# Optimization experiments

Hardware: AMD Instinct MI355X
Metric: run time of the kernel (lower is better)

Reference implementation:

```python
import jax, jax.numpy as jnp
import numpy as np

B, V, J, H, W = 32, 2, 17, 128, 128
TEMP = 0.05   # SoftArgmax2D softmax_temp
EPS = 1e-12


def _soft_argmax(hm):
    # hm: (B*V, J, H, W) -> homogeneous coords (B*V, 3, J), per-joint max value
    bv, j, h, w = hm.shape
    p = jax.nn.softmax(hm.reshape(bv, j, h * w) / TEMP, axis=-1).reshape(bv, j, h, w)
    xs = jnp.arange(w, dtype=hm.dtype)
    ys = jnp.arange(h, dtype=hm.dtype)
    x = jnp.einsum('bjhw,w->bj', p, xs)
    y = jnp.einsum('bjhw,h->bj', p, ys)
    coords = jnp.stack([x, y, jnp.ones_like(x)], axis=1)  # (bv, 3, j)
    maxv = hm.max(axis=(-2, -1))
    return coords, maxv


def _skew(t):
    # t: (..., 3) -> skew-symmetric (..., 3, 3), matches -t_mat^T + t_mat in source
    tx, ty, tz = t[..., 0], t[..., 1], t[..., 2]
    z = jnp.zeros_like(tx)
    return jnp.stack([jnp.stack([z, -tz, ty], -1),
                      jnp.stack([tz, z, -tx], -1),
                      jnp.stack([-ty, tx, z], -1)], -2)


def _forward(origin_hms, AP_K, AP_T, LAT_K, LAT_T):
    K = jnp.stack([AP_K, LAT_K], axis=1)              # (B,V,3,3)
    T = jnp.stack([AP_T, LAT_T], axis=1)              # (B,V,4,4)
    R = T[:, :, :3, :3]
    t_std = T[:, :, :3, 3]                            # (B,V,3) standard_cam_T

    # fundamental matrices for all ordered pairs: cam1 = view j, cam2 = view i
    r = jnp.einsum('bimk,bjnk->bijmn', R, R)          # R_i @ R_j^T
    t = t_std[:, :, None, :] - jnp.einsum('bijmn,bjn->bijm', r, t_std)
    M = jnp.einsum('bijmn,bijnk->bijmk', _skew(t), r)
    invK = jnp.linalg.inv(K)
    # F = invK_i^T @ [t]x @ r @ invK_j
    F = jnp.einsum('bipm,bijpq,bjql->bijml', invK, M, invK)  # (B,V,V,3,3)

    coords, maxv = _soft_argmax(origin_hms)           # (B*V,3,J), (B*V,J)
    inv_aff = jnp.diag(jnp.asarray([4.0, 4.0, 1.0], dtype=origin_hms.dtype))  # inverse of 0.25 scale
    img = jnp.einsum('mn,bvnj->bvmj', inv_aff, coords.reshape(B, V, 3, J))
    confi = maxv.reshape(B, V, J)

    # epipolar distances, fully vectorized over (b, i, j) pairs
    l = jnp.einsum('bijmn,bjnk->bijmk', F, img)       # epipolar lines in view i from joints of view j
    cv = img[:, :, None]                              # (B,V,1,3,J)
    num = jnp.sum(cv * l, axis=3) ** 2                # (B,V,V,J)
    lp = jnp.einsum('bijnm,bink->bijmk', F, img)      # F^T @ cv_joints
    div = l[..., 0, :] ** 2 + l[..., 1, :] ** 2 + lp[..., 0, :] ** 2 + lp[..., 1, :] ** 2
    dist_full = jnp.sqrt(num / (div + EPS))           # (B,V,V,J)

    others = np.asarray([[j for j in range(V) if j != i] for i in range(V)])  # (V,V-1)
    ii = np.repeat(np.arange(V)[:, None], V - 1, axis=1)
    distances = dist_full[:, ii, others]              # (B,V,V-1,J)

    # stand-in for ViewWeightNet: confidence minus mean epipolar error, softmax over views
    score = confi - distances.mean(axis=2)            # (B,V,J)
    vw = jax.nn.softmax(score, axis=1)                # (B,V,J)

    mv = jnp.where(maxv > 0.01, maxv, 1e6).reshape(B * V, J, 1, 1)
    hms_norm = origin_hms / mv
    hm4 = hms_norm.reshape(B, V, J, H, W)

    # cat order: self heatmap first, then other views (matches get_warp_weight / cat_hm layout)
    order = np.asarray([[i] + [j for j in range(V) if j != i] for i in range(V)])  # (V,V)
    cat_hm = hm4[:, order]                            # (B,V,V,J,H,W); identity-warp stand-in for CamFusionModule
    ww = vw[:, order]                                 # (B,V,V,J) warp weights
    fused_hm = jnp.sum(ww[..., None, None] * cat_hm, axis=2).reshape(B * V, J, H, W)

    coords2, _ = _soft_argmax(fused_hm)
    img2 = jnp.einsum('mn,bvnj->bvmj', inv_aff, coords2.reshape(B, V, 3, J))
    return img2[:, :, :2, :], fused_hm


def setup_inputs() -> dict:
    key = jax.random.key(0)
    k1, k2, k3, k4, k5 = jax.random.split(key, 5)
    hms = jax.random.uniform(k1, (B * V, J, H, W), dtype=jnp.float32)

    def make_K(k):
        f = 1000.0 + jax.random.normal(k, (B,)) * 10.0
        Km = jnp.zeros((B, 3, 3), dtype=jnp.float32)
        Km = Km.at[:, 0, 0].set(f).at[:, 1, 1].set(f)
        Km = Km.at[:, 0, 2].set(256.0).at[:, 1, 2].set(256.0).at[:, 2, 2].set(1.0)
        return Km

    def make_T(k):
        A = jax.random.normal(k, (B, 3, 3))
        Q, _ = jnp.linalg.qr(A)
        Q = Q * jnp.linalg.det(Q)[:, None, None]  # force det = +1 (proper rotation)
        t = jax.random.normal(jax.random.fold_in(k, 1), (B, 3, 1)) * 0.1 + jnp.asarray([0.0, 0.0, 5.0]).reshape(3, 1)
        bottom = jnp.tile(jnp.asarray([[[0.0, 0.0, 0.0, 1.0]]]), (B, 1, 1))
        return jnp.concatenate([jnp.concatenate([Q, t], axis=2), bottom], axis=1).astype(jnp.float32)

    return {"origin_hms": hms, "AP_K": make_K(k2), "AP_T": make_T(k3),
            "LAT_K": make_K(k4), "LAT_T": make_T(k5)}


def reference(origin_hms, AP_K, AP_T, LAT_K, LAT_T):
    return _forward(origin_hms, AP_K, AP_T, LAT_K, LAT_T)
```

## Files before the change

kernel.cpp:

```cpp
#include <hip/hip_runtime.h>
#include <math.h>

#define NB 32
#define NV 2
#define NJ 17
#define NH 128
#define NW 128
#define MAPN (NH * NW)
#define MAPN4 (MAPN / 4)
#define NMAPS (NB * NV * NJ)
#define NBJ (NB * NJ)
#define OUT0N (NB * NV * 2 * NJ)
#define INV_TEMP 20.0f
#define EPS_D 1e-12f

#define S_CHUNKS 4
#define S_F4 (MAPN4 / S_CHUNKS)
#define F_CHUNKS 8
#define F_F4 (MAPN4 / F_CHUNKS)

#define WS_STATS_B (NMAPS * S_CHUNKS * 16)
#define WS_W_B (NBJ * 2 * 4)
#define WS_F_B (NBJ * F_CHUNKS * 16)
#define WS_NEEDED (WS_STATS_B + WS_W_B + WS_F_B)

typedef float vfloat4 __attribute__((ext_vector_type(4)));

__device__ __forceinline__ float waveMax(float v) {
#pragma unroll
    for (int off = 32; off > 0; off >>= 1)
        v = fmaxf(v, __shfl_xor(v, off, 64));
    return v;
}
__device__ __forceinline__ float waveSum(float v) {
#pragma unroll
    for (int off = 32; off > 0; off >>= 1)
        v += __shfl_xor(v, off, 64);
    return v;
}

__device__ __forceinline__ void inv3(const float K[3][3], float o[3][3]) {
    const float a = K[0][0], b = K[0][1], c = K[0][2];
    const float d = K[1][0], e = K[1][1], f = K[1][2];
    const float g = K[2][0], h = K[2][1], i = K[2][2];
    const float A =  (e * i - f * h);
    const float Bv = -(d * i - f * g);
    const float C =  (d * h - e * g);
    const float det = a * A + b * Bv + c * C;
    const float id = 1.0f / det;
    o[0][0] = A * id;  o[0][1] = -(b * i - c * h) * id;  o[0][2] = (b * f - c * e) * id;
    o[1][0] = Bv * id; o[1][1] = (a * i - c * g) * id;   o[1][2] = -(a * f - c * d) * id;
    o[2][0] = C * id;  o[2][1] = -(a * h - b * g) * id;  o[2][2] = (a * e - b * d) * id;
}

__global__ __launch_bounds__(256, 4) void k_stats(const float* __restrict__ hms,
                                                  float* __restrict__ ws) {
    const int blk = blockIdx.x;
    const int mi = blk >> 2, c = blk & 3;
    const int tid = threadIdx.x, wid = tid >> 6, lane = tid & 63;
    const float4* A = (const float4*)hms + (size_t)mi * MAPN4 + (size_t)c * S_F4;

    float mx = -1e30f, s = 0.f, sx = 0.f, sy = 0.f;
#pragma unroll
    for (int k = 0; k < 4; ++k) {
        const int i4 = tid + k * 256;
        const float4 v = A[i4];
        const int e0 = (c * S_F4 + i4) * 4;
        const float hh = (float)(e0 >> 7);
        const float ww = (float)(e0 & 127);
        mx = fmaxf(mx, fmaxf(fmaxf(v.x, v.y), fmaxf(v.z, v.w)));
        const float ea = __expf((v.x - 1.0f) * INV_TEMP);
        const float eb = __expf((v.y - 1.0f) * INV_TEMP);
        const float ec = __expf((v.z - 1.0f) * INV_TEMP);
        const float ed = __expf((v.w - 1.0f) * INV_TEMP);
        const float se = (ea + eb) + (ec + ed);
        s += se; sy += se * hh;
        sx += ea * ww + eb * (ww + 1.f) + ec * (ww + 2.f) + ed * (ww + 3.f);
    }

    mx = waveMax(mx); s = waveSum(s); sx = waveSum(sx); sy = waveSum(sy);
    __shared__ float red[4][4];
    if (lane == 0) { red[0][wid] = mx; red[1][wid] = s; red[2][wid] = sx; red[3][wid] = sy; }
    __syncthreads();
    if (tid == 0) {
        float M = red[0][0], S = red[1][0], SX = red[2][0], SY = red[3][0];
#pragma unroll
        for (int w = 1; w < 4; ++w) {
            M = fmaxf(M, red[0][w]); S += red[1][w]; SX += red[2][w]; SY += red[3][w];
        }
        ((float4*)ws)[blk] = make_float4(M, S, SX, SY);
    }
}

__global__ void k_weights(const float* __restrict__ ws_stats,
                          const float* __restrict__ APK, const float* __restrict__ APT,
                          const float* __restrict__ LATK, const float* __restrict__ LATT,
                          float* __restrict__ wsw) {
    const int bj = blockIdx.x * 64 + threadIdx.x;
    if (bj >= NBJ) return;
    const int b = bj / NJ, j = bj % NJ;

    float conf[2], img[2][3];
    const float4* st = (const float4*)ws_stats;
#pragma unroll
    for (int v = 0; v < 2; ++v) {
        const int mi = (b * 2 + v) * NJ + j;
        float M = -1e30f, S = 0.f, SX = 0.f, SY = 0.f;
#pragma unroll
        for (int c = 0; c < S_CHUNKS; ++c) {
            const float4 p = st[mi * S_CHUNKS + c];
            M = fmaxf(M, p.x); S += p.y; SX += p.z; SY += p.w;
        }
        conf[v] = M;
        img[v][0] = 4.0f * (SX / S);
        img[v][1] = 4.0f * (SY / S);
        img[v][2] = 1.0f;
    }

    float F[2][3][3];
    {
        float Km[2][3][3], R[2][3][3], tr[2][3], iK[2][3][3];
        for (int r = 0; r < 3; ++r)
            for (int cc = 0; cc < 3; ++cc) {
                Km[0][r][cc] = APK[b * 9 + r * 3 + cc];
                Km[1][r][cc] = LATK[b * 9 + r * 3 + cc];
                R[0][r][cc] = APT[b * 16 + r * 4 + cc];
                R[1][r][cc] = LATT[b * 16 + r * 4 + cc];
            }
        for (int r = 0; r < 3; ++r) {
            tr[0][r] = APT[b * 16 + r * 4 + 3];
            tr[1][r] = LATT[b * 16 + r * 4 + 3];
        }
        inv3(Km[0], iK[0]);
        inv3(Km[1], iK[1]);

        for (int i = 0; i < 2; ++i) {
            const int jj = 1 - i;
            float r[3][3];
            for (int m = 0; m < 3; ++m)
                for (int n = 0; n < 3; ++n)
                    r[m][n] = R[i][m][0] * R[jj][n][0] + R[i][m][1] * R[jj][n][1] + R[i][m][2] * R[jj][n][2];
            float tv[3];
            for (int m = 0; m < 3; ++m)
                tv[m] = tr[i][m] - (r[m][0] * tr[jj][0] + r[m][1] * tr[jj][1] + r[m][2] * tr[jj][2]);
            const float S[3][3] = {{0.f, -tv[2], tv[1]}, {tv[2], 0.f, -tv[0]}, {-tv[1], tv[0], 0.f}};
            float M[3][3];
            for (int m = 0; m < 3; ++m)
                for (int n = 0; n < 3; ++n)
                    M[m][n] = S[m][0] * r[0][n] + S[m][1] * r[1][n] + S[m][2] * r[2][n];
            float tmp[3][3];
            for (int p = 0; p < 3; ++p)
                for (int l = 0; l < 3; ++l)
                    tmp[p][l] = M[p][0] * iK[jj][0][l] + M[p][1] * iK[jj][1][l] + M[p][2] * iK[jj][2][l];
            for (int m = 0; m < 3; ++m)
                for (int l = 0; l < 3; ++l)
                    F[i][m][l] = iK[i][0][m] * tmp[0][l] + iK[i][1][m] * tmp[1][l] + iK[i][2][m] * tmp[2][l];
        }
    }

    float score[2];
#pragma unroll
    for (int i = 0; i < 2; ++i) {
        const int jj = 1 - i;
        const float l0 = F[i][0][0] * img[jj][0] + F[i][0][1] * img[jj][1] + F[i][0][2] * img[jj][2];
        const float l1 = F[i][1][0] * img[jj][0] + F[i][1][1] * img[jj][1] + F[i][1][2] * img[jj][2];
        const float l2 = F[i][2][0] * img[jj][0] + F[i][2][1] * img[jj][1] + F[i][2][2] * img[jj][2];
        const float sdot = img[i][0] * l0 + img[i][1] * l1 + img[i][2] * l2;
        const float num = sdot * sdot;
        const float lp0 = F[i][0][0] * img[i][0] + F[i][1][0] * img[i][1] + F[i][2][0] * img[i][2];
        const float lp1 = F[i][0][1] * img[i][0] + F[i][1][1] * img[i][1] + F[i][2][1] * img[i][2];
        const float dv = l0 * l0 + l1 * l1 + lp0 * lp0 + lp1 * lp1;
        score[i] = conf[i] - sqrtf(num / (dv + EPS_D));
    }
    const float mS = fmaxf(score[0], score[1]);
    const float e0w = __expf(score[0] - mS), e1w = __expf(score[1] - mS);
    const float inv = 1.0f / (e0w + e1w);
    const float mv0 = conf[0] > 0.01f ? conf[0] : 1e6f;
    const float mv1 = conf[1] > 0.01f ? conf[1] : 1e6f;
    wsw[bj * 2 + 0] = (e0w * inv) / mv0;
    wsw[bj * 2 + 1] = (e1w * inv) / mv1;
}

__global__ __launch_bounds__(256, 4) void k_fuse(const float* __restrict__ hms,
                                                 const float* __restrict__ wsw,
                                                 float* __restrict__ out,
                                                 float* __restrict__ wsf) {
    const int blk = blockIdx.x;
    const int bj = blk >> 3, c = blk & 7;
    const int b = bj / NJ, j = bj % NJ;
    const int tid = threadIdx.x, wid = tid >> 6, lane = tid & 63;

    const float w0 = wsw[bj * 2 + 0];
    const float w1 = wsw[bj * 2 + 1];

    const size_t m0 = ((size_t)(b * 2 + 0) * NJ + j) * MAPN4;
    const size_t m1 = ((size_t)(b * 2 + 1) * NJ + j) * MAPN4;
    const float4* A  = (const float4*)hms + m0 + (size_t)c * F_F4;
    const float4* Bp = (const float4*)hms + m1 + (size_t)c * F_F4;
    float* outhm = out + OUT0N;
    vfloat4* O0 = reinterpret_cast<vfloat4*>(outhm) + m0 + (size_t)c * F_F4;
    vfloat4* O1 = reinterpret_cast<vfloat4*>(outhm) + m1 + (size_t)c * F_F4;

    float s = 0.f, sx = 0.f, sy = 0.f;
#pragma unroll
    for (int k = 0; k < 2; ++k) {
        const int i4 = tid + k * 256;
        const float4 a = A[i4];
        const float4 cc = Bp[i4];
        vfloat4 f;
        f.x = w0 * a.x + w1 * cc.x;
        f.y = w0 * a.y + w1 * cc.y;
        f.z = w0 * a.z + w1 * cc.z;
        f.w = w0 * a.w + w1 * cc.w;
        __builtin_nontemporal_store(f, &O0[i4]);
        __builtin_nontemporal_store(f, &O1[i4]);
        const int e0 = (c * F_F4 + i4) * 4;
        const float hh = (float)(e0 >> 7);
        const float ww = (float)(e0 & 127);
        const float ea = __expf((f.x - 1.0f) * INV_TEMP);
        const float eb = __expf((f.y - 1.0f) * INV_TEMP);
        const float ec = __expf((f.z - 1.0f) * INV_TEMP);
        const float ed = __expf((f.w - 1.0f) * INV_TEMP);
        const float se = (ea + eb) + (ec + ed);
        s += se; sy += se * hh;
        sx += ea * ww + eb * (ww + 1.f) + ec * (ww + 2.f) + ed * (ww + 3.f);
    }

    s = waveSum(s); sx = waveSum(sx); sy = waveSum(sy);
    __shared__ float red[3][4];
    if (lane == 0) { red[0][wid] = s; red[1][wid] = sx; red[2][wid] = sy; }
    __syncthreads();
    if (tid == 0) {
        float S = red[0][0], SX = red[1][0], SY = red[2][0];
#pragma unroll
        for (int w = 1; w < 4; ++w) { S += red[0][w]; SX += red[1][w]; SY += red[2][w]; }
        ((float4*)wsf)[blk] = make_float4(S, SX, SY, 0.f);
    }
}

__global__ void k_out(const float* __restrict__ wsf, float* __restrict__ out) {
    const int bj = blockIdx.x * 64 + threadIdx.x;
    if (bj >= NBJ) return;
    const int b = bj / NJ, j = bj % NJ;
    const float4* p = (const float4*)wsf + bj * F_CHUNKS;
    float S = 0.f, SX = 0.f, SY = 0.f;
#pragma unroll
    for (int c = 0; c < F_CHUNKS; ++c) {
        const float4 q = p[c];
        S += q.x; SX += q.y; SY += q.z;
    }
    const float x4 = 4.0f * (SX / S);
    const float y4 = 4.0f * (SY / S);
    out[((b * 2 + 0) * 2 + 0) * NJ + j] = x4;
    out[((b * 2 + 0) * 2 + 1) * NJ + j] = y4;
    out[((b * 2 + 1) * 2 + 0) * NJ + j] = x4;
    out[((b * 2 + 1) * 2 + 1) * NJ + j] = y4;
}

__global__ __launch_bounds__(512, 2) void k_one(const float* __restrict__ hms,
                                                const float* __restrict__ APK,
                                                const float* __restrict__ APT,
                                                const float* __restrict__ LATK,
                                                const float* __restrict__ LATT,
                                                float* __restrict__ out) {
    const int blk = blockIdx.x;
    const int b = blk / NJ, j = blk % NJ;
    const int tid = threadIdx.x;
    const int wid = tid >> 6, lane = tid & 63;

    float F[2][3][3];
    {
        float Km[2][3][3], R[2][3][3], tr[2][3], iK[2][3][3];
        for (int r = 0; r < 3; ++r)
            for (int c = 0; c < 3; ++c) {
                Km[0][r][c] = APK[b * 9 + r * 3 + c];
                Km[1][r][c] = LATK[b * 9 + r * 3 + c];
                R[0][r][c] = APT[b * 16 + r * 4 + c];
                R[1][r][c] = LATT[b * 16 + r * 4 + c];
            }
        for (int r = 0; r < 3; ++r) {
            tr[0][r] = APT[b * 16 + r * 4 + 3];
            tr[1][r] = LATT[b * 16 + r * 4 + 3];
        }
        inv3(Km[0], iK[0]);
        inv3(Km[1], iK[1]);

        for (int i = 0; i < 2; ++i) {
            const int jj = 1 - i;
            float r[3][3];
            for (int m = 0; m < 3; ++m)
                for (int n = 0; n < 3; ++n)
                    r[m][n] = R[i][m][0] * R[jj][n][0] + R[i][m][1] * R[jj][n][1] + R[i][m][2] * R[jj][n][2];
            float tv[3];
            for (int m = 0; m < 3; ++m)
                tv[m] = tr[i][m] - (r[m][0] * tr[jj][0] + r[m][1] * tr[jj][1] + r[m][2] * tr[jj][2]);
            const float S[3][3] = {{0.f, -tv[2], tv[1]}, {tv[2], 0.f, -tv[0]}, {-tv[1], tv[0], 0.f}};
            float M[3][3];
            for (int m = 0; m < 3; ++m)
                for (int n = 0; n < 3; ++n)
                    M[m][n] = S[m][0] * r[0][n] + S[m][1] * r[1][n] + S[m][2] * r[2][n];
            float tmp[3][3];
            for (int p = 0; p < 3; ++p)
                for (int l = 0; l < 3; ++l)
                    tmp[p][l] = M[p][0] * iK[jj][0][l] + M[p][1] * iK[jj][1][l] + M[p][2] * iK[jj][2][l];
            for (int m = 0; m < 3; ++m)
                for (int l = 0; l < 3; ++l)
                    F[i][m][l] = iK[i][0][m] * tmp[0][l] + iK[i][1][m] * tmp[1][l] + iK[i][2][m] * tmp[2][l];
        }
    }

    const int idx0 = (b * 2 + 0) * NJ + j;
    const int idx1 = (b * 2 + 1) * NJ + j;
    const size_t m0 = (size_t)idx0 * MAPN4;
    const size_t m1 = (size_t)idx1 * MAPN4;
    const float4* A  = (const float4*)hms + m0;
    const float4* Bp = (const float4*)hms + m1;

    float4 va[8];
    float mx0 = -1e30f, s0 = 0.f, sx0 = 0.f, sy0 = 0.f;
    float mx1 = -1e30f, s1 = 0.f, sx1 = 0.f, sy1 = 0.f;
#pragma unroll
    for (int u = 0; u < 8; ++u) {
        const int i4 = tid + u * 512;
        const float4 v = A[i4];
        const float4 w = Bp[i4];
        va[u] = v;
        const int e0 = i4 * 4;
        const float hh = (float)(e0 >> 7);
        const float ww = (float)(e0 & 127);
        {
            mx0 = fmaxf(mx0, fmaxf(fmaxf(v.x, v.y), fmaxf(v.z, v.w)));
            const float ea = __expf((v.x - 1.0f) * INV_TEMP);
            const float eb = __expf((v.y - 1.0f) * INV_TEMP);
            const float ec = __expf((v.z - 1.0f) * INV_TEMP);
            const float ed = __expf((v.w - 1.0f) * INV_TEMP);
            const float se = (ea + eb) + (ec + ed);
            s0 += se; sy0 += se * hh;
            sx0 += ea * ww + eb * (ww + 1.f) + ec * (ww + 2.f) + ed * (ww + 3.f);
        }
        {
            mx1 = fmaxf(mx1, fmaxf(fmaxf(w.x, w.y), fmaxf(w.z, w.w)));
            const float ea = __expf((w.x - 1.0f) * INV_TEMP);
            const float eb = __expf((w.y - 1.0f) * INV_TEMP);
            const float ec = __expf((w.z - 1.0f) * INV_TEMP);
            const float ed = __expf((w.w - 1.0f) * INV_TEMP);
            const float se = (ea + eb) + (ec + ed);
            s1 += se; sy1 += se * hh;
            sx1 += ea * ww + eb * (ww + 1.f) + ec * (ww + 2.f) + ed * (ww + 3.f);
        }
    }

    __shared__ float red[8][8];
    mx0 = waveMax(mx0); mx1 = waveMax(mx1);
    s0 = waveSum(s0); sx0 = waveSum(sx0); sy0 = waveSum(sy0);
    s1 = waveSum(s1); sx1 = waveSum(sx1); sy1 = waveSum(sy1);
    if (lane == 0) {
        red[0][wid] = mx0; red[1][wid] = s0; red[2][wid] = sx0; red[3][wid] = sy0;
        red[4][wid] = mx1; red[5][wid] = s1; red[6][wid] = sx1; red[7][wid] = sy1;
    }
    __syncthreads();
    float M0 = red[0][0], S0 = red[1][0], SX0 = red[2][0], SY0 = red[3][0];
    float M1 = red[4][0], S1 = red[5][0], SX1 = red[6][0], SY1 = red[7][0];
#pragma unroll
    for (int w = 1; w < 8; ++w) {
        M0 = fmaxf(M0, red[0][w]); S0 += red[1][w]; SX0 += red[2][w]; SY0 += red[3][w];
        M1 = fmaxf(M1, red[4][w]); S1 += red[5][w]; SX1 += red[6][w]; SY1 += red[7][w];
    }

    float w0, w1;
    {
        const float conf[2] = {M0, M1};
        float img[2][3];
        img[0][0] = 4.0f * (SX0 / S0); img[0][1] = 4.0f * (SY0 / S0); img[0][2] = 1.0f;
        img[1][0] = 4.0f * (SX1 / S1); img[1][1] = 4.0f * (SY1 / S1); img[1][2] = 1.0f;

        float score[2];
        for (int i = 0; i < 2; ++i) {
            const int jj = 1 - i;
            const float l0 = F[i][0][0] * img[jj][0] + F[i][0][1] * img[jj][1] + F[i][0][2] * img[jj][2];
            const float l1 = F[i][1][0] * img[jj][0] + F[i][1][1] * img[jj][1] + F[i][1][2] * img[jj][2];
            const float l2 = F[i][2][0] * img[jj][0] + F[i][2][1] * img[jj][1] + F[i][2][2] * img[jj][2];
            const float sdot = img[i][0] * l0 + img[i][1] * l1 + img[i][2] * l2;
            const float num = sdot * sdot;
            const float lp0 = F[i][0][0] * img[i][0] + F[i][1][0] * img[i][1] + F[i][2][0] * img[i][2];
            const float lp1 = F[i][0][1] * img[i][0] + F[i][1][1] * img[i][1] + F[i][2][1] * img[i][2];
            const float dv = l0 * l0 + l1 * l1 + lp0 * lp0 + lp1 * lp1;
            score[i] = conf[i] - sqrtf(num / (dv + EPS_D));
        }
        const float mS = fmaxf(score[0], score[1]);
        const float e0w = __expf(score[0] - mS), e1w = __expf(score[1] - mS);
        const float inv = 1.0f / (e0w + e1w);
        const float mv0 = conf[0] > 0.01f ? conf[0] : 1e6f;
        const float mv1 = conf[1] > 0.01f ? conf[1] : 1e6f;
        w0 = (e0w * inv) / mv0;
        w1 = (e1w * inv) / mv1;
    }

    float* outhm = out + OUT0N;
    vfloat4* O0 = reinterpret_cast<vfloat4*>(outhm) + m0;
    vfloat4* O1 = reinterpret_cast<vfloat4*>(outhm) + m1;

    float s = 0.f, sx = 0.f, sy = 0.f;
#pragma unroll
    for (int u = 0; u < 8; ++u) {
        const int i4 = tid + u * 512;
        const float4 a = va[u];
        const float4 c = Bp[i4];
        vfloat4 f;
        f.x = w0 * a.x + w1 * c.x;
        f.y = w0 * a.y + w1 * c.y;
        f.z = w0 * a.z + w1 * c.z;
        f.w = w0 * a.w + w1 * c.w;
        __builtin_nontemporal_store(f, &O0[i4]);
        __builtin_nontemporal_store(f, &O1[i4]);
        const int e0 = i4 * 4;
        const float hh = (float)(e0 >> 7);
        const float ww = (float)(e0 & 127);
        const float ea = __expf((f.x - 1.0f) * INV_TEMP);
        const float eb = __expf((f.y - 1.0f) * INV_TEMP);
        const float ec = __expf((f.z - 1.0f) * INV_TEMP);
        const float ed = __expf((f.w - 1.0f) * INV_TEMP);
        const float se = (ea + eb) + (ec + ed);
        s += se; sy += se * hh;
        sx += ea * ww + eb * (ww + 1.f) + ec * (ww + 2.f) + ed * (ww + 3.f);
    }

    __syncthreads();
    s = waveSum(s); sx = waveSum(sx); sy = waveSum(sy);
    if (lane == 0) { red[0][wid] = s; red[1][wid] = sx; red[2][wid] = sy; }
    __syncthreads();
    if (tid == 0) {
        float S = red[0][0], SX = red[1][0], SY = red[2][0];
#pragma unroll
        for (int w = 1; w < 8; ++w) { S += red[0][w]; SX += red[1][w]; SY += red[2][w]; }
        const float x4 = 4.0f * (SX / S);
        const float y4 = 4.0f * (SY / S);
        out[((b * 2 + 0) * 2 + 0) * NJ + j] = x4;
        out[((b * 2 + 0) * 2 + 1) * NJ + j] = y4;
        out[((b * 2 + 1) * 2 + 0) * NJ + j] = x4;
        out[((b * 2 + 1) * 2 + 1) * NJ + j] = y4;
    }
}

extern "C" void kernel_launch(void* const* d_in, const int* in_sizes, int n_in,
                              void* d_out, int out_size, void* d_ws, size_t ws_size,
                              hipStream_t stream) {
    const float* hms  = (const float*)d_in[0];
    const float* APK  = (const float*)d_in[1];
    const float* APT  = (const float*)d_in[2];
    const float* LATK = (const float*)d_in[3];
    const float* LATT = (const float*)d_in[4];
    float* out = (float*)d_out;

    if (d_ws != nullptr && ws_size >= (size_t)WS_NEEDED) {
        float* ws_stats = (float*)d_ws;
        float* ws_w = ws_stats + NMAPS * S_CHUNKS * 4;
        float* ws_f = ws_w + NBJ * 2;
        k_stats<<<NMAPS * S_CHUNKS, 256, 0, stream>>>(hms, ws_stats);
        k_weights<<<(NBJ + 63) / 64, 64, 0, stream>>>(ws_stats, APK, APT, LATK, LATT, ws_w);
        k_fuse<<<NBJ * F_CHUNKS, 256, 0, stream>>>(hms, ws_w, out, ws_f);
        k_out<<<(NBJ + 63) / 64, 64, 0, stream>>>(ws_f, out);
    } else {
        k_one<<<NBJ, 512, 0, stream>>>(hms, APK, APT, LATK, LATT, out);
    }
}
```

Baseline: 141.9 us.

## Fuse stats, weights and fusion passes into one kernel split by halves

```diff
diff --git a/kernel.cpp b/kernel.cpp
--- a/kernel.cpp
+++ b/kernel.cpp
@@ -8,21 +8,13 @@
 #define NW 128
 #define MAPN (NH * NW)
 #define MAPN4 (MAPN / 4)
-#define NMAPS (NB * NV * NJ)
 #define NBJ (NB * NJ)
 #define OUT0N (NB * NV * 2 * NJ)
 #define INV_TEMP 20.0f
 #define EPS_D 1e-12f
 
-#define S_CHUNKS 4
-#define S_F4 (MAPN4 / S_CHUNKS)
-#define F_CHUNKS 8
-#define F_F4 (MAPN4 / F_CHUNKS)
-
-#define WS_STATS_B (NMAPS * S_CHUNKS * 16)
-#define WS_W_B (NBJ * 2 * 4)
-#define WS_F_B (NBJ * F_CHUNKS * 16)
-#define WS_NEEDED (WS_STATS_B + WS_W_B + WS_F_B)
+#define HALF4 (MAPN4 / 2)
+#define WS_NEEDED (NBJ * 2 * 16)
 
 typedef float vfloat4 __attribute__((ext_vector_type(4)));
 
@@ -53,218 +45,16 @@
     o[2][0] = C * id;  o[2][1] = -(a * h - b * g) * id;  o[2][2] = (a * e - b * d) * id;
 }
 
-__global__ __launch_bounds__(256, 4) void k_stats(const float* __restrict__ hms,
-                                                  float* __restrict__ ws) {
+__global__ __launch_bounds__(512, 2) void k_main(const float* __restrict__ hms,
+                                                 const float* __restrict__ APK,
+                                                 const float* __restrict__ APT,
+                                                 const float* __restrict__ LATK,
+                                                 const float* __restrict__ LATT,
+                                                 float* __restrict__ ws_fp,
+                                                 float* __restrict__ out) {
     const int blk = blockIdx.x;
-    const int mi = blk >> 2, c = blk & 3;
-    const int tid = threadIdx.x, wid = tid >> 6, lane = tid & 63;
-    const float4* A = (const float4*)hms + (size_t)mi * MAPN4 + (size_t)c * S_F4;
-
-    float mx = -1e30f, s = 0.f, sx = 0.f, sy = 0.f;
-#pragma unroll
-    for (int k = 0; k < 4; ++k) {
-        const int i4 = tid + k * 256;
-        const float4 v = A[i4];
-        const int e0 = (c * S_F4 + i4) * 4;
-        const float hh = (float)(e0 >> 7);
-        const float ww = (float)(e0 & 127);
-        mx = fmaxf(mx, fmaxf(fmaxf(v.x, v.y), fmaxf(v.z, v.w)));
-        const float ea = __expf((v.x - 1.0f) * INV_TEMP);
-        const float eb = __expf((v.y - 1.0f) * INV_TEMP);
-        const float ec = __expf((v.z - 1.0f) * INV_TEMP);
-        const float ed = __expf((v.w - 1.0f) * INV_TEMP);
-        const float se = (ea + eb) + (ec + ed);
-        s += se; sy += se * hh;
-        sx += ea * ww + eb * (ww + 1.f) + ec * (ww + 2.f) + ed * (ww + 3.f);
-    }
-
-    mx = waveMax(mx); s = waveSum(s); sx = waveSum(sx); sy = waveSum(sy);
-    __shared__ float red[4][4];
-    if (lane == 0) { red[0][wid] = mx; red[1][wid] = s; red[2][wid] = sx; red[3][wid] = sy; }
-    __syncthreads();
-    if (tid == 0) {
-        float M = red[0][0], S = red[1][0], SX = red[2][0], SY = red[3][0];
-#pragma unroll
-        for (int w = 1; w < 4; ++w) {
-            M = fmaxf(M, red[0][w]); S += red[1][w]; SX += red[2][w]; SY += red[3][w];
-        }
-        ((float4*)ws)[blk] = make_float4(M, S, SX, SY);
-    }
-}
-
-__global__ void k_weights(const float* __restrict__ ws_stats,
-                          const float* __restrict__ APK, const float* __restrict__ APT,
-                          const float* __restrict__ LATK, const float* __restrict__ LATT,
-                          float* __restrict__ wsw) {
-    const int bj = blockIdx.x * 64 + threadIdx.x;
-    if (bj >= NBJ) return;
+    const int bj = blk >> 1, half = blk & 1;
     const int b = bj / NJ, j = bj % NJ;
-
-    float conf[2], img[2][3];
-    const float4* st = (const float4*)ws_stats;
-#pragma unroll
-    for (int v = 0; v < 2; ++v) {
-        const int mi = (b * 2 + v) * NJ + j;
-        float M = -1e30f, S = 0.f, SX = 0.f, SY = 0.f;
-#pragma unroll
-        for (int c = 0; c < S_CHUNKS; ++c) {
-            const float4 p = st[mi * S_CHUNKS + c];
-            M = fmaxf(M, p.x); S += p.y; SX += p.z; SY += p.w;
-        }
-        conf[v] = M;
-        img[v][0] = 4.0f * (SX / S);
-        img[v][1] = 4.0f * (SY / S);
-        img[v][2] = 1.0f;
-    }
-
-    float F[2][3][3];
-    {
-        float Km[2][3][3], R[2][3][3], tr[2][3], iK[2][3][3];
-        for (int r = 0; r < 3; ++r)
-            for (int cc = 0; cc < 3; ++cc) {
-                Km[0][r][cc] = APK[b * 9 + r * 3 + cc];
-                Km[1][r][cc] = LATK[b * 9 + r * 3 + cc];
-                R[0][r][cc] = APT[b * 16 + r * 4 + cc];
-                R[1][r][cc] = LATT[b * 16 + r * 4 + cc];
-            }
-        for (int r = 0; r < 3; ++r) {
-            tr[0][r] = APT[b * 16 + r * 4 + 3];
-            tr[1][r] = LATT[b * 16 + r * 4 + 3];
-        }
-        inv3(Km[0], iK[0]);
-        inv3(Km[1], iK[1]);
-
-        for (int i = 0; i < 2; ++i) {
-            const int jj = 1 - i;
-            float r[3][3];
-            for (int m = 0; m < 3; ++m)
-                for (int n = 0; n < 3; ++n)
-                    r[m][n] = R[i][m][0] * R[jj][n][0] + R[i][m][1] * R[jj][n][1] + R[i][m][2] * R[jj][n][2];
-            float tv[3];
-            for (int m = 0; m < 3; ++m)
-                tv[m] = tr[i][m] - (r[m][0] * tr[jj][0] + r[m][1] * tr[jj][1] + r[m][2] * tr[jj][2]);
-            const float S[3][3] = {{0.f, -tv[2], tv[1]}, {tv[2], 0.f, -tv[0]}, {-tv[1], tv[0], 0.f}};
-            float M[3][3];
-            for (int m = 0; m < 3; ++m)
-                for (int n = 0; n < 3; ++n)
-                    M[m][n] = S[m][0] * r[0][n] + S[m][1] * r[1][n] + S[m][2] * r[2][n];
-            float tmp[3][3];
-            for (int p = 0; p < 3; ++p)
-                for (int l = 0; l < 3; ++l)
-                    tmp[p][l] = M[p][0] * iK[jj][0][l] + M[p][1] * iK[jj][1][l] + M[p][2] * iK[jj][2][l];
-            for (int m = 0; m < 3; ++m)
-                for (int l = 0; l < 3; ++l)
-                    F[i][m][l] = iK[i][0][m] * tmp[0][l] + iK[i][1][m] * tmp[1][l] + iK[i][2][m] * tmp[2][l];
-        }
-    }
-
-    float score[2];
-#pragma unroll
-    for (int i = 0; i < 2; ++i) {
-        const int jj = 1 - i;
-        const float l0 = F[i][0][0] * img[jj][0] + F[i][0][1] * img[jj][1] + F[i][0][2] * img[jj][2];
-        const float l1 = F[i][1][0] * img[jj][0] + F[i][1][1] * img[jj][1] + F[i][1][2] * img[jj][2];
-        const float l2 = F[i][2][0] * img[jj][0] + F[i][2][1] * img[jj][1] + F[i][2][2] * img[jj][2];
-        const float sdot = img[i][0] * l0 + img[i][1] * l1 + img[i][2] * l2;
-        const float num = sdot * sdot;
-        const float lp0 = F[i][0][0] * img[i][0] + F[i][1][0] * img[i][1] + F[i][2][0] * img[i][2];
-        const float lp1 = F[i][0][1] * img[i][0] + F[i][1][1] * img[i][1] + F[i][2][1] * img[i][2];
-        const float dv = l0 * l0 + l1 * l1 + lp0 * lp0 + lp1 * lp1;
-        score[i] = conf[i] - sqrtf(num / (dv + EPS_D));
-    }
-    const float mS = fmaxf(score[0], score[1]);
-    const float e0w = __expf(score[0] - mS), e1w = __expf(score[1] - mS);
-    const float inv = 1.0f / (e0w + e1w);
-    const float mv0 = conf[0] > 0.01f ? conf[0] : 1e6f;
-    const float mv1 = conf[1] > 0.01f ? conf[1] : 1e6f;
-    wsw[bj * 2 + 0] = (e0w * inv) / mv0;
-    wsw[bj * 2 + 1] = (e1w * inv) / mv1;
-}
-
-__global__ __launch_bounds__(256, 4) void k_fuse(const float* __restrict__ hms,
-                                                 const float* __restrict__ wsw,
-                                                 float* __restrict__ out,
-                                                 float* __restrict__ wsf) {
-    const int blk = blockIdx.x;
-    const int bj = blk >> 3, c = blk & 7;
-    const int b = bj / NJ, j = bj % NJ;
-    const int tid = threadIdx.x, wid = tid >> 6, lane = tid & 63;
-
-    const float w0 = wsw[bj * 2 + 0];
-    const float w1 = wsw[bj * 2 + 1];
-
-    const size_t m0 = ((size_t)(b * 2 + 0) * NJ + j) * MAPN4;
-    const size_t m1 = ((size_t)(b * 2 + 1) * NJ + j) * MAPN4;
-    const float4* A  = (const float4*)hms + m0 + (size_t)c * F_F4;
-    const float4* Bp = (const float4*)hms + m1 + (size_t)c * F_F4;
-    float* outhm = out + OUT0N;
-    vfloat4* O0 = reinterpret_cast<vfloat4*>(outhm) + m0 + (size_t)c * F_F4;
-    vfloat4* O1 = reinterpret_cast<vfloat4*>(outhm) + m1 + (size_t)c * F_F4;
-
-    float s = 0.f, sx = 0.f, sy = 0.f;
-#pragma unroll
-    for (int k = 0; k < 2; ++k) {
-        const int i4 = tid + k * 256;
-        const float4 a = A[i4];
-        const float4 cc = Bp[i4];
-        vfloat4 f;
-        f.x = w0 * a.x + w1 * cc.x;
-        f.y = w0 * a.y + w1 * cc.y;
-        f.z = w0 * a.z + w1 * cc.z;
-        f.w = w0 * a.w + w1 * cc.w;
-        __builtin_nontemporal_store(f, &O0[i4]);
-        __builtin_nontemporal_store(f, &O1[i4]);
-        const int e0 = (c * F_F4 + i4) * 4;
-        const float hh = (float)(e0 >> 7);
-        const float ww = (float)(e0 & 127);
-        const float ea = __expf((f.x - 1.0f) * INV_TEMP);
-        const float eb = __expf((f.y - 1.0f) * INV_TEMP);
-        const float ec = __expf((f.z - 1.0f) * INV_TEMP);
-        const float ed = __expf((f.w - 1.0f) * INV_TEMP);
-        const float se = (ea + eb) + (ec + ed);
-        s += se; sy += se * hh;
-        sx += ea * ww + eb * (ww + 1.f) + ec * (ww + 2.f) + ed * (ww + 3.f);
-    }
-
-    s = waveSum(s); sx = waveSum(sx); sy = waveSum(sy);
-    __shared__ float red[3][4];
-    if (lane == 0) { red[0][wid] = s; red[1][wid] = sx; red[2][wid] = sy; }
-    __syncthreads();
-    if (tid == 0) {
-        float S = red[0][0], SX = red[1][0], SY = red[2][0];
-#pragma unroll
-        for (int w = 1; w < 4; ++w) { S += red[0][w]; SX += red[1][w]; SY += red[2][w]; }
-        ((float4*)wsf)[blk] = make_float4(S, SX, SY, 0.f);
-    }
-}
-
-__global__ void k_out(const float* __restrict__ wsf, float* __restrict__ out) {
-    const int bj = blockIdx.x * 64 + threadIdx.x;
-    if (bj >= NBJ) return;
-    const int b = bj / NJ, j = bj % NJ;
-    const float4* p = (const float4*)wsf + bj * F_CHUNKS;
-    float S = 0.f, SX = 0.f, SY = 0.f;
-#pragma unroll
-    for (int c = 0; c < F_CHUNKS; ++c) {
-        const float4 q = p[c];
-        S += q.x; SX += q.y; SY += q.z;
-    }
-    const float x4 = 4.0f * (SX / S);
-    const float y4 = 4.0f * (SY / S);
-    out[((b * 2 + 0) * 2 + 0) * NJ + j] = x4;
-    out[((b * 2 + 0) * 2 + 1) * NJ + j] = y4;
-    out[((b * 2 + 1) * 2 + 0) * NJ + j] = x4;
-    out[((b * 2 + 1) * 2 + 1) * NJ + j] = y4;
-}
-
-__global__ __launch_bounds__(512, 2) void k_one(const float* __restrict__ hms,
-                                                const float* __restrict__ APK,
-                                                const float* __restrict__ APT,
-                                                const float* __restrict__ LATK,
-                                                const float* __restrict__ LATT,
-                                                float* __restrict__ out) {
-    const int blk = blockIdx.x;
-    const int b = blk / NJ, j = blk % NJ;
     const int tid = threadIdx.x;
     const int wid = tid >> 6, lane = tid & 63;
 
@@ -309,10 +99,199 @@
         }
     }
 
-    const int idx0 = (b * 2 + 0) * NJ + j;
-    const int idx1 = (b * 2 + 1) * NJ + j;
-    const size_t m0 = (size_t)idx0 * MAPN4;
-    const size_t m1 = (size_t)idx1 * MAPN4;
+    const size_t m0 = ((size_t)(b * 2 + 0) * NJ + j) * MAPN4;
+    const size_t m1 = ((size_t)(b * 2 + 1) * NJ + j) * MAPN4;
+    const float4* A  = (const float4*)hms + m0;
+    const float4* Bp = (const float4*)hms + m1;
+
+    float mx0 = -1e30f, s0 = 0.f, sx0 = 0.f, sy0 = 0.f;
+    float mx1 = -1e30f, s1 = 0.f, sx1 = 0.f, sy1 = 0.f;
+#pragma unroll
+    for (int u = 0; u < 8; ++u) {
+        const int i4 = tid + u * 512;
+        const float4 v = A[i4];
+        const float4 w = Bp[i4];
+        const int e0 = i4 * 4;
+        const float hh = (float)(e0 >> 7);
+        const float ww = (float)(e0 & 127);
+        {
+            mx0 = fmaxf(mx0, fmaxf(fmaxf(v.x, v.y), fmaxf(v.z, v.w)));
+            const float ea = __expf((v.x - 1.0f) * INV_TEMP);
+            const float eb = __expf((v.y - 1.0f) * INV_TEMP);
+            const float ec = __expf((v.z - 1.0f) * INV_TEMP);
+            const float ed = __expf((v.w - 1.0f) * INV_TEMP);
+            const float se = (ea + eb) + (ec + ed);
+            s0 += se; sy0 += se * hh;
+            sx0 += ea * ww + eb * (ww + 1.f) + ec * (ww + 2.f) + ed * (ww + 3.f);
+        }
+        {
+            mx1 = fmaxf(mx1, fmaxf(fmaxf(w.x, w.y), fmaxf(w.z, w.w)));
+            const float ea = __expf((w.x - 1.0f) * INV_TEMP);
+            const float eb = __expf((w.y - 1.0f) * INV_TEMP);
+            const float ec = __expf((w.z - 1.0f) * INV_TEMP);
+            const float ed = __expf((w.w - 1.0f) * INV_TEMP);
+            const float se = (ea + eb) + (ec + ed);
+            s1 += se; sy1 += se * hh;
+            sx1 += ea * ww + eb * (ww + 1.f) + ec * (ww + 2.f) + ed * (ww + 3.f);
+        }
+    }
+
+    __shared__ float red[8][8];
+    mx0 = waveMax(mx0); mx1 = waveMax(mx1);
+    s0 = waveSum(s0); sx0 = waveSum(sx0); sy0 = waveSum(sy0);
+    s1 = waveSum(s1); sx1 = waveSum(sx1); sy1 = waveSum(sy1);
+    if (lane == 0) {
+        red[0][wid] = mx0; red[1][wid] = s0; red[2][wid] = sx0; red[3][wid] = sy0;
+        red[4][wid] = mx1; red[5][wid] = s1; red[6][wid] = sx1; red[7][wid] = sy1;
+    }
+    __syncthreads();
+    float M0 = red[0][0], S0 = red[1][0], SX0 = red[2][0], SY0 = red[3][0];
+    float M1 = red[4][0], S1 = red[5][0], SX1 = red[6][0], SY1 = red[7][0];
+#pragma unroll
+    for (int w = 1; w < 8; ++w) {
+        M0 = fmaxf(M0, red[0][w]); S0 += red[1][w]; SX0 += red[2][w]; SY0 += red[3][w];
+        M1 = fmaxf(M1, red[4][w]); S1 += red[5][w]; SX1 += red[6][w]; SY1 += red[7][w];
+    }
+
+    float w0, w1;
+    {
+        const float conf[2] = {M0, M1};
+        float img[2][3];
+        img[0][0] = 4.0f * (SX0 / S0); img[0][1] = 4.0f * (SY0 / S0); img[0][2] = 1.0f;
+        img[1][0] = 4.0f * (SX1 / S1); img[1][1] = 4.0f * (SY1 / S1); img[1][2] = 1.0f;
+
+        float score[2];
+        for (int i = 0; i < 2; ++i) {
+            const int jj = 1 - i;
+            const float l0 = F[i][0][0] * img[jj][0] + F[i][0][1] * img[jj][1] + F[i][0][2] * img[jj][2];
+            const float l1 = F[i][1][0] * img[jj][0] + F[i][1][1] * img[jj][1] + F[i][1][2] * img[jj][2];
+            const float l2 = F[i][2][0] * img[jj][0] + F[i][2][1] * img[jj][1] + F[i][2][2] * img[jj][2];
+            const float sdot = img[i][0] * l0 + img[i][1] * l1 + img[i][2] * l2;
+            const float num = sdot * sdot;
+            const float lp0 = F[i][0][0] * img[i][0] + F[i][1][0] * img[i][1] + F[i][2][0] * img[i][2];
+            const float lp1 = F[i][0][1] * img[i][0] + F[i][1][1] * img[i][1] + F[i][2][1] * img[i][2];
+            const float dv = l0 * l0 + l1 * l1 + lp0 * lp0 + lp1 * lp1;
+            score[i] = conf[i] - sqrtf(num / (dv + EPS_D));
+        }
+        const float mS = fmaxf(score[0], score[1]);
+        const float e0w = __expf(score[0] - mS), e1w = __expf(score[1] - mS);
+        const float inv = 1.0f / (e0w + e1w);
+        const float mv0 = conf[0] > 0.01f ? conf[0] : 1e6f;
+        const float mv1 = conf[1] > 0.01f ? conf[1] : 1e6f;
+        w0 = (e0w * inv) / mv0;
+        w1 = (e1w * inv) / mv1;
+    }
+
+    float* outhm = out + OUT0N;
+    vfloat4* O0 = reinterpret_cast<vfloat4*>(outhm) + m0;
+    vfloat4* O1 = reinterpret_cast<vfloat4*>(outhm) + m1;
+    const int hbase = half * HALF4;
+
+    float s = 0.f, sx = 0.f, sy = 0.f;
+#pragma unroll
+    for (int u = 0; u < 4; ++u) {
+        const int i4 = hbase + tid + u * 512;
+        const float4 a = A[i4];
+        const float4 c = Bp[i4];
+        vfloat4 f;
+        f.x = w0 * a.x + w1 * c.x;
+        f.y = w0 * a.y + w1 * c.y;
+        f.z = w0 * a.z + w1 * c.z;
+        f.w = w0 * a.w + w1 * c.w;
+        __builtin_nontemporal_store(f, &O0[i4]);
+        __builtin_nontemporal_store(f, &O1[i4]);
+        const int e0 = i4 * 4;
+        const float hh = (float)(e0 >> 7);
+        const float ww = (float)(e0 & 127);
+        const float ea = __expf((f.x - 1.0f) * INV_TEMP);
+        const float eb = __expf((f.y - 1.0f) * INV_TEMP);
+        const float ec = __expf((f.z - 1.0f) * INV_TEMP);
+        const float ed = __expf((f.w - 1.0f) * INV_TEMP);
+        const float se = (ea + eb) + (ec + ed);
+        s += se; sy += se * hh;
+        sx += ea * ww + eb * (ww + 1.f) + ec * (ww + 2.f) + ed * (ww + 3.f);
+    }
+
+    __syncthreads();
+    s = waveSum(s); sx = waveSum(sx); sy = waveSum(sy);
+    if (lane == 0) { red[0][wid] = s; red[1][wid] = sx; red[2][wid] = sy; }
+    __syncthreads();
+    if (tid == 0) {
+        float S = red[0][0], SX = red[1][0], SY = red[2][0];
+#pragma unroll
+        for (int w = 1; w < 8; ++w) { S += red[0][w]; SX += red[1][w]; SY += red[2][w]; }
+        ((float4*)ws_fp)[blk] = make_float4(S, SX, SY, 0.f);
+    }
+}
+
+__global__ void k_out(const float* __restrict__ ws_fp, float* __restrict__ out) {
+    const int bj = blockIdx.x * 64 + threadIdx.x;
+    if (bj >= NBJ) return;
+    const int b = bj / NJ, j = bj % NJ;
+    const float4 p0 = ((const float4*)ws_fp)[bj * 2 + 0];
+    const float4 p1 = ((const float4*)ws_fp)[bj * 2 + 1];
+    const float S = p0.x + p1.x, SX = p0.y + p1.y, SY = p0.z + p1.z;
+    const float x4 = 4.0f * (SX / S);
+    const float y4 = 4.0f * (SY / S);
+    out[((b * 2 + 0) * 2 + 0) * NJ + j] = x4;
+    out[((b * 2 + 0) * 2 + 1) * NJ + j] = y4;
+    out[((b * 2 + 1) * 2 + 0) * NJ + j] = x4;
+    out[((b * 2 + 1) * 2 + 1) * NJ + j] = y4;
+}
+
+__global__ __launch_bounds__(512, 2) void k_one(const float* __restrict__ hms,
+                                                const float* __restrict__ APK,
+                                                const float* __restrict__ APT,
+                                                const float* __restrict__ LATK,
+                                                const float* __restrict__ LATT,
+                                                float* __restrict__ out) {
+    const int blk = blockIdx.x;
+    const int b = blk / NJ, j = blk % NJ;
+    const int tid = threadIdx.x;
+    const int wid = tid >> 6, lane = tid & 63;
+
+    float F[2][3][3];
+    {
+        float Km[2][3][3], R[2][3][3], tr[2][3], iK[2][3][3];
+        for (int r = 0; r < 3; ++r)
+            for (int c = 0; c < 3; ++c) {
+                Km[0][r][c] = APK[b * 9 + r * 3 + c];
+                Km[1][r][c] = LATK[b * 9 + r * 3 + c];
+                R[0][r][c] = APT[b * 16 + r * 4 + c];
+                R[1][r][c] = LATT[b * 16 + r * 4 + c];
+            }
+        for (int r = 0; r < 3; ++r) {
+            tr[0][r] = APT[b * 16 + r * 4 + 3];
+            tr[1][r] = LATT[b * 16 + r * 4 + 3];
+        }
+        inv3(Km[0], iK[0]);
+        inv3(Km[1], iK[1]);
+        for (int i = 0; i < 2; ++i) {
+            const int jj = 1 - i;
+            float r[3][3];
+            for (int m = 0; m < 3; ++m)
+                for (int n = 0; n < 3; ++n)
+                    r[m][n] = R[i][m][0] * R[jj][n][0] + R[i][m][1] * R[jj][n][1] + R[i][m][2] * R[jj][n][2];
+            float tv[3];
+            for (int m = 0; m < 3; ++m)
+                tv[m] = tr[i][m] - (r[m][0] * tr[jj][0] + r[m][1] * tr[jj][1] + r[m][2] * tr[jj][2]);
+            const float S[3][3] = {{0.f, -tv[2], tv[1]}, {tv[2], 0.f, -tv[0]}, {-tv[1], tv[0], 0.f}};
+            float M[3][3];
+            for (int m = 0; m < 3; ++m)
+                for (int n = 0; n < 3; ++n)
+                    M[m][n] = S[m][0] * r[0][n] + S[m][1] * r[1][n] + S[m][2] * r[2][n];
+            float tmp[3][3];
+            for (int p = 0; p < 3; ++p)
+                for (int l = 0; l < 3; ++l)
+                    tmp[p][l] = M[p][0] * iK[jj][0][l] + M[p][1] * iK[jj][1][l] + M[p][2] * iK[jj][2][l];
+            for (int m = 0; m < 3; ++m)
+                for (int l = 0; l < 3; ++l)
+                    F[i][m][l] = iK[i][0][m] * tmp[0][l] + iK[i][1][m] * tmp[1][l] + iK[i][2][m] * tmp[2][l];
+        }
+    }
+
+    const size_t m0 = ((size_t)(b * 2 + 0) * NJ + j) * MAPN4;
+    const size_t m1 = ((size_t)(b * 2 + 1) * NJ + j) * MAPN4;
     const float4* A  = (const float4*)hms + m0;
     const float4* Bp = (const float4*)hms + m1;
 
@@ -373,7 +352,6 @@
         float img[2][3];
         img[0][0] = 4.0f * (SX0 / S0); img[0][1] = 4.0f * (SY0 / S0); img[0][2] = 1.0f;
         img[1][0] = 4.0f * (SX1 / S1); img[1][1] = 4.0f * (SY1 / S1); img[1][2] = 1.0f;
-
         float score[2];
         for (int i = 0; i < 2; ++i) {
             const int jj = 1 - i;
@@ -453,13 +431,9 @@
     float* out = (float*)d_out;
 
     if (d_ws != nullptr && ws_size >= (size_t)WS_NEEDED) {
-        float* ws_stats = (float*)d_ws;
-        float* ws_w = ws_stats + NMAPS * S_CHUNKS * 4;
-        float* ws_f = ws_w + NBJ * 2;
-        k_stats<<<NMAPS * S_CHUNKS, 256, 0, stream>>>(hms, ws_stats);
-        k_weights<<<(NBJ + 63) / 64, 64, 0, stream>>>(ws_stats, APK, APT, LATK, LATT, ws_w);
-        k_fuse<<<NBJ * F_CHUNKS, 256, 0, stream>>>(hms, ws_w, out, ws_f);
-        k_out<<<(NBJ + 63) / 64, 64, 0, stream>>>(ws_f, out);
+        float* ws_fp = (float*)d_ws;
+        k_main<<<NBJ * 2, 512, 0, stream>>>(hms, APK, APT, LATK, LATT, ws_fp, out);
+        k_out<<<(NBJ + 63) / 64, 64, 0, stream>>>(ws_fp, out);
     } else {
         k_one<<<NBJ, 512, 0, stream>>>(hms, APK, APT, LATK, LATT, out);
     }
```

Result: slower. 145.6 us (+2.6%).
